# Kernel optimization log

Hardware: AMD Instinct MI355X
Metric: run time of the kernel (lower is better)

Reference implementation:

```python
import jax, jax.numpy as jnp
from jax import lax
import numpy as np

RATIOS = (0.5, 1.0, 2.0)
SCALES = (8, 16, 32)
BASE = 16
STRIDE = 16
IMG_H, IMG_W = 1024, 1024
NMS_THR = 0.7
N_IN = 6000   # eval mode (training=False)
N_OUT = 300
MIN_SIZE = 16


def _base_anchors():
    ctr = BASE / 2.0
    anc = []
    for r in RATIOS:
        for s in SCALES:
            h = BASE * s * np.sqrt(r)
            w = BASE * s * np.sqrt(1.0 / r)
            anc.append([ctr - h / 2, ctr - w / 2, ctr + h / 2, ctr + w / 2])
    return np.asarray(anc, dtype=np.float32)  # (9,4) yxyx


def _shifted_anchors(H, W):
    base = _base_anchors()
    sy = np.arange(H, dtype=np.float32) * STRIDE
    sx = np.arange(W, dtype=np.float32) * STRIDE
    yy, xx = np.meshgrid(sy, sx, indexing='ij')
    shift = np.stack([yy, xx, yy, xx], axis=-1).reshape(-1, 1, 4)  # (H*W,1,4)
    return jnp.asarray((shift + base[None]).reshape(-1, 4))        # (H*W*9,4)


def _conv(x, w, b):
    y = lax.conv_general_dilated(x, w, (1, 1), 'SAME',
                                 dimension_numbers=('NCHW', 'OIHW', 'NCHW'))
    return y + b[None, :, None, None]


def _loc2bbox(src, locs):
    h = src[:, 2] - src[:, 0]
    w = src[:, 3] - src[:, 1]
    cy = src[:, 0] + 0.5 * h
    cx = src[:, 1] + 0.5 * w
    dy, dx, dh, dw = locs[:, 0], locs[:, 1], locs[:, 2], locs[:, 3]
    cty = dy * h + cy
    ctx = dx * w + cx
    th = jnp.exp(dh) * h
    tw = jnp.exp(dw) * w
    return jnp.stack([cty - 0.5 * th, ctx - 0.5 * tw,
                      cty + 0.5 * th, ctx + 0.5 * tw], axis=-1)


def _nms_keep(boxes, valid):
    n = boxes.shape[0]
    areas = (boxes[:, 2] - boxes[:, 0]) * (boxes[:, 3] - boxes[:, 1])
    idx = jnp.arange(n)

    def body(i, keep):
        b = lax.dynamic_slice(boxes, (i, 0), (1, 4))[0]
        yy1 = jnp.maximum(b[0], boxes[:, 0])
        xx1 = jnp.maximum(b[1], boxes[:, 1])
        yy2 = jnp.minimum(b[2], boxes[:, 2])
        xx2 = jnp.minimum(b[3], boxes[:, 3])
        inter = jnp.clip(yy2 - yy1, 0) * jnp.clip(xx2 - xx1, 0)
        iou = inter / (areas[i] + areas - inter + 1e-9)
        sup = (iou > NMS_THR) & (idx > i) & keep[i]
        return keep & ~sup

    return lax.fori_loop(0, n, body, valid)


def _proposals(locs, fg, anchors):
    # locs (R,4), fg (R,), anchors (R,4) -> (N_OUT,4) padded with zeros
    rois = _loc2bbox(anchors, locs)
    y1 = jnp.clip(rois[:, 0], 0, IMG_H)
    y2 = jnp.clip(rois[:, 2], 0, IMG_H)
    x1 = jnp.clip(rois[:, 1], 0, IMG_W)
    x2 = jnp.clip(rois[:, 3], 0, IMG_W)
    rois = jnp.stack([y1, x1, y2, x2], axis=-1)
    valid = ((y2 - y1) >= MIN_SIZE) & ((x2 - x1) >= MIN_SIZE)
    s = jnp.where(valid, fg, -jnp.inf)
    order = jnp.argsort(-s)[:N_IN]
    rois_s = rois[order]
    valid_s = valid[order]
    keep = _nms_keep(rois_s, valid_s)
    rank = jnp.cumsum(keep.astype(jnp.int32)) - 1
    tgt = jnp.where(keep & (rank < N_OUT), rank, N_OUT)
    out = jnp.zeros((N_OUT + 1, 4), rois.dtype).at[tgt].set(rois_s)
    return out[:N_OUT]


def reference(x, conv_w, conv_b, score_w, score_b, loc_w, loc_b):
    B, C, H, W = x.shape
    anchors = _shifted_anchors(H, W)                      # (R,4)
    h = jax.nn.relu(_conv(x, conv_w, conv_b))             # (B,mid,H,W)
    rpn_locs = _conv(h, loc_w, loc_b).transpose(0, 2, 3, 1).reshape(B, -1, 4)
    rpn_scores = _conv(h, score_w, score_b).transpose(0, 2, 3, 1).reshape(B, -1, 2)
    fg = jax.nn.softmax(rpn_scores, axis=2)[:, :, 1]      # (B,R)
    rois = jax.vmap(_proposals, in_axes=(0, 0, None))(rpn_locs, fg, anchors)
    rois = rois.reshape(-1, 4)                            # (B*N_OUT,4)
    roi_indices = jnp.repeat(jnp.arange(B, dtype=jnp.int32), N_OUT)
    return rpn_scores, rpn_locs, rois, roi_indices, anchors


def setup_inputs() -> dict:
    key = jax.random.key(0)
    ks = jax.random.split(key, 7)
    B, Cin, Cmid, H, W = 4, 512, 512, 64, 64
    return {
        'x': jax.random.normal(ks[0], (B, Cin, H, W), jnp.float32),
        'conv_w': jax.random.normal(ks[1], (Cmid, Cin, 3, 3), jnp.float32) * 0.01,
        'conv_b': jax.random.normal(ks[2], (Cmid,), jnp.float32) * 0.01,
        'score_w': jax.random.normal(ks[3], (18, Cmid, 1, 1), jnp.float32) * 0.01,
        'score_b': jax.random.normal(ks[4], (18,), jnp.float32) * 0.01,
        'loc_w': jax.random.normal(ks[5], (36, Cmid, 1, 1), jnp.float32) * 0.01,
        'loc_b': jax.random.normal(ks[6], (36,), jnp.float32) * 0.01,
    }
```

## Files before the change

### kernel.cpp

```cpp
#include <hip/hip_runtime.h>
#include <cstdint>
#include <cmath>

namespace {
constexpr int BATCH = 4;
constexpr int CIN   = 512;
constexpr int CMID  = 512;
constexpr int HSZ   = 64, WSZ = 64, HWP = 4096;
constexpr int NA    = 36864;
constexpr int NIN_  = 6000;
constexpr int NOUT2 = 300;
constexpr int NW    = 94;

constexpr size_t O_SC  = 0;
constexpr size_t O_LC  = 294912;
constexpr size_t O_ROI = 884736;
constexpr size_t O_IDX = 889536;
constexpr size_t O_ANC = 890736;

constexpr size_t W_H    = 0;
constexpr size_t W_WHI  = 8388608;
constexpr size_t W_XSP  = 10747904;
constexpr size_t W_END_PS = 19136512;
constexpr size_t W_R4   = 0;
constexpr size_t W_SK   = 589824;
constexpr size_t W_CNT  = 753664;
constexpr size_t W_GH0  = 753728;
constexpr size_t W_GH1  = 770112;
constexpr size_t W_CT0  = 786496;
constexpr size_t W_CKEY = 901184;
constexpr size_t W_RS   = 1196096;
constexpr size_t W_VS   = 1292096;
constexpr size_t W_MAT  = 1316096;
}

typedef _Float16 f16;
typedef __attribute__((ext_vector_type(4))) _Float16 f16x4;
typedef __attribute__((ext_vector_type(8))) _Float16 f16x8;
typedef __attribute__((ext_vector_type(4))) float f32x4;

__global__ __launch_bounds__(256) void k0w(const float* __restrict__ w,
                                           f16* __restrict__ gw2) {
    int g = blockIdx.x * 256 + threadIdx.x;
    int lane = g & 63;
    int t1 = g >> 6;
    int hl = t1 & 1;
    int nt = (t1 >> 1) & 3;
    int wc = (t1 >> 3) & 1;
    int cg = (t1 >> 4) & 3;
    int ck = t1 >> 6;
    int kk = ck % 9;
    int chunk = ck / 9;
    int co  = cg * 128 + wc * 64 + nt * 16 + (lane & 15);
    int ci0 = chunk * 32 + (lane >> 4) * 8;
    f16x8 o;
#pragma unroll
    for (int e = 0; e < 8; ++e) {
        float f = w[((size_t)co * CIN + ci0 + e) * 9 + kk] * 64.0f;
        f16 hv = (f16)f;
        o[e] = hl ? (f16)((f - (float)hv) * 2048.0f) : hv;
    }
    *(f16x8*)&gw2[(size_t)g * 8] = o;
}

__global__ __launch_bounds__(256) void k0x(const float* __restrict__ x,
                                           f16* __restrict__ xsp) {
    const int pt = blockIdx.x, ch = blockIdx.y, b = blockIdx.z, t = threadIdx.x;
    __shared__ float ld[32 * 261];
    const int px0 = pt * 256;
    const int lpx = (t & 63) * 4, lc0 = t >> 6;
#pragma unroll
    for (int r = 0; r < 8; ++r) {
        int ci = r * 4 + lc0;
        float4 v = *(const float4*)&x[((size_t)(b * 512 + ch * 32 + ci)) * 4096 + px0 + lpx];
        float* d = &ld[ci * 261 + lpx];
        d[0] = v.x; d[1] = v.y; d[2] = v.z; d[3] = v.w;
    }
    __syncthreads();
    size_t ob = ((size_t)(b * 16 + ch) * 4096 + px0 + t) * 64;
#pragma unroll
    for (int cqx = 0; cqx < 8; ++cqx) {
        f16x8 o;
#pragma unroll
        for (int i = 0; i < 4; ++i) {
            float f = ld[(cqx * 4 + i) * 261 + t];
            f16 hf = (f16)f;
            o[i]     = hf;
            o[4 + i] = (f16)((f - (float)hf) * 2048.0f);
        }
        *(f16x8*)&xsp[ob + cqx * 8] = o;
    }
}

template <bool PS>
__global__ __launch_bounds__(256, 2) void k1_mfma(const float* __restrict__ x,
                                                  const f16* __restrict__ xsp,
                                                  const f16* __restrict__ gw2,
                                                  const float* __restrict__ bias,
                                                  float* __restrict__ h) {
    const int pt = blockIdx.x, cg = blockIdx.y, b = blockIdx.z;
    const int y0 = pt * 2, co0 = cg * 128;
    const int t = threadIdx.x;
    const int wave = t >> 6, lane = t & 63;
    const int wp = wave >> 1, wc = wave & 1;
    const int m = lane & 15, q = lane >> 4;

    __shared__ __align__(16) f16 xs[2][4 * 66 * 40];

    f32x4 acc1[2][2][4], acc2[2][2][4];
#pragma unroll
    for (int r = 0; r < 2; ++r)
#pragma unroll
        for (int j = 0; j < 2; ++j)
#pragma unroll
            for (int n = 0; n < 4; ++n) { acc1[r][j][n] = (f32x4)0.0f; acc2[r][j][n] = (f32x4)0.0f; }

    const int cq = t & 7, srow = (t >> 3) & 3, cseg = t >> 5;
    const int gy = y0 - 1 + srow;
    const bool yok = (gy >= 0 && gy < HSZ);

    if (t < 128) {
        int buf = t >> 6, rr = (t >> 4) & 3, cc = ((t >> 3) & 1) ? 65 : 0, cq2 = t & 7;
        f16x4 z = (f16x4)(f16)0.0f;
        *(f16x4*)&xs[buf][(rr * 66 + cc) * 40 + cq2 * 4] = z;
    }

    const size_t wlanebase = (size_t)(cg * 2 + wc) * 4096 + (size_t)lane * 8;

    f16x8 xv[8];
    if (PS) {
        const f16* xb = xsp + (((size_t)(b * 16 + 0) * 4096 + (size_t)(yok ? gy : 0) * 64) * 64);
#pragma unroll
        for (int jj = 0; jj < 8; ++jj) {
            int c = (jj + cq) & 7;
            xv[jj] = (f16x8)(f16)0.0f;
            if (yok) xv[jj] = *(const f16x8*)&xb[(size_t)(cseg * 8 + c) * 64 + cq * 8];
        }
    }

    for (int chunk = 0; chunk < 16; ++chunk) {
        __syncthreads();
        if (PS) {
#pragma unroll
            for (int jj = 0; jj < 8; ++jj) {
                int c = (jj + cq) & 7;
                int col = cseg * 8 + c + 1;
                f16x8 v = xv[jj];
                int base = (srow * 66 + col) * 40 + cq * 4;
                *(f16x4*)&xs[0][base] = __builtin_shufflevector(v, v, 0, 1, 2, 3);
                *(f16x4*)&xs[1][base] = __builtin_shufflevector(v, v, 4, 5, 6, 7);
            }
        } else {
            float vbuf[4][8];
            const float* xp = x + ((size_t)(b * CIN + chunk * 32 + cq * 4)) * HWP + gy * WSZ + cseg * 8;
#pragma unroll
            for (int i = 0; i < 4; ++i) {
                if (yok) {
                    float4 u0 = *(const float4*)(xp + (size_t)i * HWP);
                    float4 u1 = *(const float4*)(xp + (size_t)i * HWP + 4);
                    vbuf[i][0] = u0.x; vbuf[i][1] = u0.y; vbuf[i][2] = u0.z; vbuf[i][3] = u0.w;
                    vbuf[i][4] = u1.x; vbuf[i][5] = u1.y; vbuf[i][6] = u1.z; vbuf[i][7] = u1.w;
                } else {
#pragma unroll
                    for (int jj = 0; jj < 8; ++jj) vbuf[i][jj] = 0.0f;
                }
            }
#pragma unroll
            for (int jj = 0; jj < 8; ++jj) {
                int c = (jj + cq) & 7;
                int col = cseg * 8 + c + 1;
                f16x4 hv, lv;
#pragma unroll
                for (int i = 0; i < 4; ++i) {
                    float f = vbuf[i][c];
                    f16 hf = (f16)f;
                    hv[i] = hf;
                    lv[i] = (f16)((f - (float)hf) * 2048.0f);
                }
                int base = (srow * 66 + col) * 40 + cq * 4;
                *(f16x4*)&xs[0][base] = hv;
                *(f16x4*)&xs[1][base] = lv;
            }
        }
        __syncthreads();

        if (PS && chunk + 1 < 16) {
            const f16* xb2 = xsp + (((size_t)(b * 16 + chunk + 1) * 4096 + (size_t)(yok ? gy : 0) * 64) * 64);
#pragma unroll
            for (int jj = 0; jj < 8; ++jj) {
                int c = (jj + cq) & 7;
                xv[jj] = (f16x8)(f16)0.0f;
                if (yok) xv[jj] = *(const f16x8*)&xb2[(size_t)(cseg * 8 + c) * 64 + cq * 8];
            }
        }

        const f16* wck = gw2 + (size_t)chunk * (9 * 32768) + wlanebase;
#pragma unroll
        for (int kk = 0; kk < 9; ++kk) {
            const int ky = (kk >= 6) ? 2 : (kk >= 3) ? 1 : 0;
            const int kx = kk - ky * 3;
            const f16* wptr = wck + (size_t)kk * 32768;
            f16x8 bh[4], bl[4];
#pragma unroll
            for (int nt = 0; nt < 4; ++nt) {
                bh[nt] = *(const f16x8*)&wptr[nt * 1024];
                bl[nt] = *(const f16x8*)&wptr[nt * 1024 + 512];
            }
            f16x8 ah[2][2], al[2][2];
#pragma unroll
            for (int r = 0; r < 2; ++r)
#pragma unroll
                for (int j = 0; j < 2; ++j) {
                    int off = ((r + ky) * 66 + (wp * 2 + j) * 16 + m + kx) * 40 + q * 8;
                    ah[r][j] = *(const f16x8*)&xs[0][off];
                    al[r][j] = *(const f16x8*)&xs[1][off];
                }
#pragma unroll
            for (int r = 0; r < 2; ++r)
#pragma unroll
                for (int j = 0; j < 2; ++j)
#pragma unroll
                    for (int nt = 0; nt < 4; ++nt) {
                        acc1[r][j][nt] = __builtin_amdgcn_mfma_f32_16x16x32_f16(ah[r][j], bh[nt], acc1[r][j][nt], 0, 0, 0);
                        acc2[r][j][nt] = __builtin_amdgcn_mfma_f32_16x16x32_f16(ah[r][j], bl[nt], acc2[r][j][nt], 0, 0, 0);
                        acc2[r][j][nt] = __builtin_amdgcn_mfma_f32_16x16x32_f16(al[r][j], bh[nt], acc2[r][j][nt], 0, 0, 0);
                    }
        }
    }

#pragma unroll
    for (int r = 0; r < 2; ++r) {
        const int y = y0 + r;
#pragma unroll
        for (int nt = 0; nt < 4; ++nt) {
            const int co = co0 + wc * 64 + nt * 16 + m;
            const float bv = bias[co];
            size_t rowbase = ((size_t)(b * CMID + co)) * HWP + y * WSZ;
#pragma unroll
            for (int j = 0; j < 2; ++j) {
                float4 o;
                o.x = fmaxf((acc1[r][j][nt][0] + acc2[r][j][nt][0] * (1.0f / 2048.0f)) * (1.0f / 64.0f) + bv, 0.0f);
                o.y = fmaxf((acc1[r][j][nt][1] + acc2[r][j][nt][1] * (1.0f / 2048.0f)) * (1.0f / 64.0f) + bv, 0.0f);
                o.z = fmaxf((acc1[r][j][nt][2] + acc2[r][j][nt][2] * (1.0f / 2048.0f)) * (1.0f / 64.0f) + bv, 0.0f);
                o.w = fmaxf((acc1[r][j][nt][3] + acc2[r][j][nt][3] * (1.0f / 2048.0f)) * (1.0f / 64.0f) + bv, 0.0f);
                *(float4*)&h[rowbase + (wp * 2 + j) * 16 + q * 4] = o;
            }
        }
    }
}

__global__ __launch_bounds__(256) void k2_conv1(const float* __restrict__ h,
                                                const float* __restrict__ sw,
                                                const float* __restrict__ sb,
                                                const float* __restrict__ lw,
                                                const float* __restrict__ lb,
                                                float* __restrict__ out) {
    const int y = blockIdx.x;
    const int b = blockIdx.y;
    const int t = threadIdx.x;
    const int c4  = (t & 15) * 4;
    const int px4 = (t >> 4) * 4;
    __shared__ __align__(16) float hs[1024];
    __shared__ __align__(16) float wsm[16 * 68];

    float acc[4][4];
#pragma unroll
    for (int i = 0; i < 4; ++i)
#pragma unroll
        for (int j = 0; j < 4; ++j) acc[i][j] = 0.f;

    const int s_px = (t & 15) * 4;
    const int s_ci = t >> 4;
    for (int ci0 = 0; ci0 < CMID; ci0 += 16) {
        *(float4*)&hs[s_ci * 64 + s_px] =
            *(const float4*)&h[((size_t)(b * CMID + ci0 + s_ci)) * HWP + y * 64 + s_px];
#pragma unroll
        for (int k = 0; k < 4; ++k) {
            int idx = k * 256 + t;
            int ci = idx & 15, c = idx >> 4;
            float v = 0.f;
            if (c < 18) v = sw[c * 512 + ci0 + ci];
            else if (c < 54) v = lw[(c - 18) * 512 + ci0 + ci];
            wsm[ci * 68 + c] = v;
        }
        __syncthreads();
#pragma unroll
        for (int ci = 0; ci < 16; ++ci) {
            float4 hv = *(const float4*)&hs[ci * 64 + px4];
            float4 wv = *(const float4*)&wsm[ci * 68 + c4];
            acc[0][0] = fmaf(wv.x, hv.x, acc[0][0]);
            acc[0][1] = fmaf(wv.x, hv.y, acc[0][1]);
            acc[0][2] = fmaf(wv.x, hv.z, acc[0][2]);
            acc[0][3] = fmaf(wv.x, hv.w, acc[0][3]);
            acc[1][0] = fmaf(wv.y, hv.x, acc[1][0]);
            acc[1][1] = fmaf(wv.y, hv.y, acc[1][1]);
            acc[1][2] = fmaf(wv.y, hv.z, acc[1][2]);
            acc[1][3] = fmaf(wv.y, hv.w, acc[1][3]);
            acc[2][0] = fmaf(wv.z, hv.x, acc[2][0]);
            acc[2][1] = fmaf(wv.z, hv.y, acc[2][1]);
            acc[2][2] = fmaf(wv.z, hv.z, acc[2][2]);
            acc[2][3] = fmaf(wv.z, hv.w, acc[2][3]);
            acc[3][0] = fmaf(wv.w, hv.x, acc[3][0]);
            acc[3][1] = fmaf(wv.w, hv.y, acc[3][1]);
            acc[3][2] = fmaf(wv.w, hv.z, acc[3][2]);
            acc[3][3] = fmaf(wv.w, hv.w, acc[3][3]);
        }
        __syncthreads();
    }

#pragma unroll
    for (int cc = 0; cc < 4; ++cc) {
        int c = c4 + cc;
        if (c >= 54) break;
        float bv = (c < 18) ? sb[c] : lb[c - 18];
#pragma unroll
        for (int pp = 0; pp < 4; ++pp) {
            int px = y * 64 + px4 + pp;
            float v = acc[cc][pp] + bv;
            if (c < 18)
                out[O_SC + (size_t)b * 73728 + (size_t)px * 18 + c] = v;
            else
                out[O_LC + (size_t)b * 147456 + (size_t)px * 36 + (c - 18)] = v;
        }
    }
}

__global__ __launch_bounds__(256) void k4z(int* __restrict__ gh,
                                           int* __restrict__ gcnt) {
    int i = blockIdx.x * 256 + threadIdx.x;
    gh[i] = 0;
    if (i < BATCH) gcnt[i] = 0;
}

__global__ __launch_bounds__(256) void k3_prop(float* __restrict__ out,
                                               float* __restrict__ rois4,
                                               float* __restrict__ skey,
                                               int* __restrict__ gh0) {
    const int t = threadIdx.x;
    const int p = blockIdx.x * 256 + t;
    const int b = blockIdx.y;
    __shared__ int lh[4096];
    for (int k = t; k < 4096; k += 256) lh[k] = 0;
    __syncthreads();
    const int px = p / 9;
    const int a  = p - px * 9;
    const int yy = px >> 6, xx = px & 63;
    const int ri = a / 3, si = a - ri * 3;
    const double rat[3] = {0.5, 1.0, 2.0};
    const double scl[3] = {8.0, 16.0, 32.0};
    double hhd = 16.0 * scl[si] * sqrt(rat[ri]);
    double wwd = 16.0 * scl[si] * sqrt(1.0 / rat[ri]);
    float a0 = (float)(8.0 - hhd / 2.0), a1 = (float)(8.0 - wwd / 2.0);
    float a2 = (float)(8.0 + hhd / 2.0), a3 = (float)(8.0 + wwd / 2.0);
    float sy = (float)(yy * 16), sx = (float)(xx * 16);
    float A0 = sy + a0, A1 = sx + a1, A2 = sy + a2, A3 = sx + a3;
    if (b == 0) {
        float4 av; av.x = A0; av.y = A1; av.z = A2; av.w = A3;
        *(float4*)&out[O_ANC + (size_t)p * 4] = av;
    }
    const float* sc = out + O_SC + (size_t)b * 73728 + (size_t)px * 18 + a * 2;
    float s0 = sc[0], s1 = sc[1];
    float mm = fmaxf(s0, s1);
    float e0 = expf(s0 - mm), e1 = expf(s1 - mm);
    float fg = e1 / (e0 + e1);
    const float* lc = out + O_LC + (size_t)b * 147456 + (size_t)px * 36 + a * 4;
    float dy = lc[0], dxv = lc[1], dh = lc[2], dwv = lc[3];
    float ah = A2 - A0, aw = A3 - A1;
    float cy = A0 + 0.5f * ah, cx = A1 + 0.5f * aw;
    float cty = dy * ah + cy, ctx = dxv * aw + cx;
    float th = expf(dh) * ah, tw = expf(dwv) * aw;
    float ry1 = cty - 0.5f * th, rx1 = ctx - 0.5f * tw;
    float ry2 = cty + 0.5f * th, rx2 = ctx + 0.5f * tw;
    float y1 = fminf(fmaxf(ry1, 0.f), 1024.f);
    float y2 = fminf(fmaxf(ry2, 0.f), 1024.f);
    float x1 = fminf(fmaxf(rx1, 0.f), 1024.f);
    float x2 = fminf(fmaxf(rx2, 0.f), 1024.f);
    bool valid = ((y2 - y1) >= 16.f) && ((x2 - x1) >= 16.f);
    float sk = valid ? fg : -__builtin_inff();
    float4 rv; rv.x = y1; rv.y = x1; rv.z = y2; rv.w = x2;
    *(float4*)&rois4[((size_t)b * NA + p) * 4] = rv;
    skey[(size_t)b * NA + p] = sk;
    unsigned uu = __float_as_uint(sk);
    uu = (uu & 0x80000000u) ? ~uu : (uu | 0x80000000u);
    atomicAdd(&lh[uu >> 20], 1);
    __syncthreads();
    for (int k = t; k < 4096; k += 256) {
        int v = lh[k];
        if (v) atomicAdd(&gh0[(size_t)b * 4096 + k], v);
    }
}

__global__ __launch_bounds__(256) void k4cut0(const int* __restrict__ gh,
                                              int* __restrict__ cut0,
                                              int* __restrict__ prev0) {
    const int b = blockIdx.x, t = threadIdx.x;
    __shared__ int hh[4096];
    __shared__ int tsum[256];
    __shared__ int s_cut, s_prev;
    for (int k = t; k < 4096; k += 256) hh[k] = gh[(size_t)b * 4096 + k];
    __syncthreads();
    int s = 0;
#pragma unroll
    for (int j = 0; j < 16; ++j) s += hh[t * 16 + j];
    tsum[t] = s;
    __syncthreads();
    if (t == 0) {
        int run = 0;
        for (int tt = 255; tt >= 0; --tt) { int tmp = tsum[tt]; tsum[tt] = run; run += tmp; }
    }
    __syncthreads();
    {
        const int target = NIN_;
        int run = tsum[t];
        for (int v = t * 16 + 15; v >= t * 16; --v) {
            int prev = run;
            run += hh[v];
            if (run >= target && prev < target) { s_cut = v; s_prev = prev; }
        }
    }
    __syncthreads();
    if (t == 0) { cut0[b] = s_cut; prev0[b] = s_prev; }
}

__global__ __launch_bounds__(256) void k4h1(const float* __restrict__ skey,
                                            const int* __restrict__ cut0,
                                            int* __restrict__ gh1,
                                            float* __restrict__ rois_s,
                                            int* __restrict__ valid_s) {
    const int b = blockIdx.y, t = threadIdx.x;
    {
        int gid = (blockIdx.y * 32 + blockIdx.x) * 256 + t;
        if (gid < BATCH * NIN_) valid_s[gid] = 0;
        for (int k = gid; k < BATCH * NIN_ * 4; k += 32768) rois_s[k] = 0.f;
    }
    __shared__ int lh[4096];
    for (int k = t; k < 4096; k += 256) lh[k] = 0;
    __syncthreads();
    const int c1 = cut0[b];
    for (int i = blockIdx.x * 256 + t; i < NA; i += 32 * 256) {
        float sk = skey[(size_t)b * NA + i];
        unsigned u = __float_as_uint(sk);
        u = (u & 0x80000000u) ? ~u : (u | 0x80000000u);
        if ((int)(u >> 20) == c1) atomicAdd(&lh[(u >> 8) & 0xFFFu], 1);
    }
    __syncthreads();
    for (int k = t; k < 4096; k += 256) {
        int v = lh[k];
        if (v) atomicAdd(&gh1[(size_t)b * 4096 + k], v);
    }
}

__global__ __launch_bounds__(256) void k4cut1(const int* __restrict__ gh,
                                              const int* __restrict__ prev0,
                                              int* __restrict__ cut1) {
    const int b = blockIdx.x, t = threadIdx.x;
    __shared__ int hh[4096];
    __shared__ int tsum[256];
    __shared__ int s_cut;
    for (int k = t; k < 4096; k += 256) hh[k] = gh[(size_t)b * 4096 + k];
    __syncthreads();
    int s = 0;
#pragma unroll
    for (int j = 0; j < 16; ++j) s += hh[t * 16 + j];
    tsum[t] = s;
    __syncthreads();
    if (t == 0) {
        int run = 0;
        for (int tt = 255; tt >= 0; --tt) { int tmp = tsum[tt]; tsum[tt] = run; run += tmp; }
    }
    __syncthreads();
    {
        const int target = NIN_ - prev0[b];
        int run = tsum[t];
        for (int v = t * 16 + 15; v >= t * 16; --v) {
            int prev = run;
            run += hh[v];
            if (run >= target && prev < target) { s_cut = v; }
        }
    }
    __syncthreads();
    if (t == 0) cut1[b] = s_cut;
}

__global__ __launch_bounds__(256) void k4cmp(const float* __restrict__ skey,
                                             const int* __restrict__ cut0,
                                             const int* __restrict__ cut1,
                                             int* __restrict__ gcnt,
                                             unsigned long long* __restrict__ ckey) {
    const int b = blockIdx.y, t = threadIdx.x;
    __shared__ unsigned long long lbuf[1280];
    __shared__ int lcnt, lbase;
    if (t == 0) lcnt = 0;
    __syncthreads();
    const int c1 = cut0[b], c2 = cut1[b];
    for (int i = blockIdx.x * 256 + t; i < NA; i += 32 * 256) {
        float sk = skey[(size_t)b * NA + i];
        unsigned u = __float_as_uint(sk);
        u = (u & 0x80000000u) ? ~u : (u | 0x80000000u);
        int b1 = (int)(u >> 20), b2 = (int)((u >> 8) & 0xFFFu);
        if (b1 > c1 || (b1 == c1 && b2 >= c2)) {
            int lp = atomicAdd(&lcnt, 1);
            lbuf[lp] = ((unsigned long long)u << 16) | (unsigned long long)(36863 - i);
        }
    }
    __syncthreads();
    if (t == 0) lbase = atomicAdd(gcnt + b, lcnt);
    __syncthreads();
    const int n = lcnt, base = lbase;
    for (int k = t; k < n; k += 256) ckey[(size_t)b * NA + base + k] = lbuf[k];
}

__global__ __launch_bounds__(256) void k4d_rank(const int* __restrict__ cnt,
                                                const unsigned long long* __restrict__ ckey,
                                                const float* __restrict__ rois4,
                                                float* __restrict__ rois_s,
                                                int* __restrict__ valid_s) {
    const int b = blockIdx.y;
    const int C = cnt[b];
    if (blockIdx.x * 256 >= C) return;
    const int gi = blockIdx.x * 256 + threadIdx.x;
    const bool act = gi < C;
    const unsigned long long mk = act ? ckey[(size_t)b * NA + gi] : 0ULL;
    __shared__ unsigned long long kl[512];
    int rank = 0;
    for (int c0 = 0; c0 < C; c0 += 512) {
        __syncthreads();
#pragma unroll
        for (int kk = 0; kk < 2; ++kk) {
            int k = threadIdx.x + kk * 256;
            int src = c0 + k;
            kl[k] = (src < C) ? ckey[(size_t)b * NA + src] : 0ULL;
        }
        __syncthreads();
        if (act) {
            int n = min(512, C - c0);
            int j = 0;
            for (; j + 4 <= n; j += 4) {
                rank += (kl[j]     > mk);
                rank += (kl[j + 1] > mk);
                rank += (kl[j + 2] > mk);
                rank += (kl[j + 3] > mk);
            }
            for (; j < n; ++j) rank += (kl[j] > mk);
        }
    }
    if (act && rank < NIN_) {
        int p = 36863 - (int)(mk & 0xFFFFull);
        const float4 bx = *(const float4*)&rois4[((size_t)b * NA + p) * 4];
        *(float4*)&rois_s[((size_t)b * NIN_ + rank) * 4] = bx;
        valid_s[b * NIN_ + rank] = ((unsigned)(mk >> 16) != 0x007FFFFFu) ? 1 : 0;
    }
}

__global__ __launch_bounds__(256) void k5_mat(const float* __restrict__ rois_s,
                                              unsigned long long* __restrict__ mat) {
    const int b = blockIdx.y, rb = blockIdx.x;
    const int t = threadIdx.x, wave = t >> 6, lane = t & 63;
    const int i = rb * 64 + lane;
    const bool rowok = (i < NIN_);
    __shared__ float cs[4][5][64];
    const float* bb = rois_s + (size_t)b * NIN_ * 4;

    float r0 = 0, r1 = 0, r2 = 0, r3 = 0, ra = 0;
    if (rowok) {
        float4 v = *(const float4*)&bb[(size_t)i * 4];
        r0 = v.x; r1 = v.y; r2 = v.z; r3 = v.w;
        ra = (v.z - v.x) * (v.w - v.y);
    }
    unsigned long long* mrow = mat + ((size_t)b * NIN_ + (size_t)(rowok ? i : 0)) * NW;

    if (rowok)
        for (int cb = wave; cb < rb; cb += 4) mrow[cb] = 0ull;

    for (int cb = rb + wave; cb < NW; cb += 4) {
        const int j0 = cb * 64;
        const int j  = j0 + lane;
        float4 v;
        if (j < NIN_) v = *(const float4*)&bb[(size_t)j * 4];
        else { v.x = 0; v.y = 0; v.z = 0; v.w = 0; }
        cs[wave][0][lane] = v.x; cs[wave][1][lane] = v.y;
        cs[wave][2][lane] = v.z; cs[wave][3][lane] = v.w;
        cs[wave][4][lane] = (v.z - v.x) * (v.w - v.y);
        unsigned long long wm = 0;
        if (rowok) {
#pragma unroll 8
            for (int k = 0; k < 64; ++k) {
                float yy1 = fmaxf(r0, cs[wave][0][k]), xx1 = fmaxf(r1, cs[wave][1][k]);
                float yy2 = fminf(r2, cs[wave][2][k]), xx2 = fminf(r3, cs[wave][3][k]);
                float inter = fmaxf(yy2 - yy1, 0.f) * fmaxf(xx2 - xx1, 0.f);
                float iou = inter / (ra + cs[wave][4][k] - inter + 1e-9f);
                int jj = j0 + k;
                if ((iou > 0.7f) && (jj > i) && (jj < NIN_)) wm |= (1ull << k);
            }
            mrow[cb] = wm;
        }
    }
}

__global__ __launch_bounds__(64) void k5_scan(const unsigned long long* __restrict__ mat,
                                              const float* __restrict__ rois_s,
                                              const int* __restrict__ valid_s,
                                              float* __restrict__ out) {
    const int b = blockIdx.x, t = threadIdx.x;
    for (int k = t; k < NOUT2 * 4; k += 64) out[O_ROI + (size_t)b * NOUT2 * 4 + k] = 0.f;
    for (int k = t; k < NOUT2; k += 64) out[O_IDX + (size_t)b * NOUT2 + k] = (float)b;

    unsigned long long A = 0, B = 0;
    for (int w = 0; w < NW; ++w) {
        int i = w * 64 + t;
        int v = (i < NIN_) ? valid_s[b * NIN_ + i] : 0;
        unsigned long long m = __ballot(v == 0);
        if (w < 64) { if (t == w) A = m; }
        else        { if (t == w - 64) B = m; }
    }

    const unsigned long long* mb = mat + (size_t)b * NIN_ * NW;
    const float* bb = rois_s + (size_t)b * NIN_ * 4;
    int kept = 0;
    for (int w = 0; w < NW && kept < NOUT2; ++w) {
        unsigned long long cur = (w < 64) ? __shfl(A, w) : __shfl(B, w - 64);
        unsigned long long avail = ~cur;
        while (avail != 0ull && kept < NOUT2) {
            int b0 = __builtin_ctzll(avail);
            unsigned long long rest = avail & (avail - 1ull);
            const int i0 = w * 64 + b0;
            const unsigned long long* row0 = mb + (size_t)i0 * NW;
            unsigned long long r0A = row0[t];
            unsigned long long r0B = (t < NW - 64) ? row0[64 + t] : 0ull;
            const bool has1 = (rest != 0ull);
            const int b1 = has1 ? __builtin_ctzll(rest) : 0;
            unsigned long long r1A = 0ull, r1B = 0ull;
            if (has1) {
                const unsigned long long* row1 = mb + (size_t)(w * 64 + b1) * NW;
                r1A = row1[t];
                r1B = (t < NW - 64) ? row1[64 + t] : 0ull;
            }
            if (t == 0) {
                float4 bx = *(const float4*)&bb[(size_t)i0 * 4];
                *(float4*)&out[O_ROI + ((size_t)b * NOUT2 + kept) * 4] = bx;
            }
            kept++;
            if (kept >= NOUT2) break;
            A |= r0A; B |= r0B;
            unsigned long long rw0 = (w < 64) ? __shfl(r0A, w) : __shfl(r0B, w - 64);
            avail &= ~rw0;
            avail &= ~(1ull << b0);
            if (has1 && (avail & (1ull << b1))) {
                if (t == 0) {
                    float4 bx = *(const float4*)&bb[(size_t)(w * 64 + b1) * 4];
                    *(float4*)&out[O_ROI + ((size_t)b * NOUT2 + kept) * 4] = bx;
                }
                kept++;
                if (kept >= NOUT2) break;
                A |= r1A; B |= r1B;
                unsigned long long rw1 = (w < 64) ? __shfl(r1A, w) : __shfl(r1B, w - 64);
                avail &= ~rw1;
                avail &= ~(1ull << b1);
            }
        }
    }
}

extern "C" void kernel_launch(void* const* d_in, const int* in_sizes, int n_in,
                              void* d_out, int out_size, void* d_ws, size_t ws_size,
                              hipStream_t stream) {
    const float* x       = (const float*)d_in[0];
    const float* conv_w  = (const float*)d_in[1];
    const float* conv_b  = (const float*)d_in[2];
    const float* score_w = (const float*)d_in[3];
    const float* score_b = (const float*)d_in[4];
    const float* loc_w   = (const float*)d_in[5];
    const float* loc_b   = (const float*)d_in[6];
    float* out = (float*)d_out;
    float* ws  = (float*)d_ws;

    f16* gw2 = (f16*)(ws + W_WHI);
    f16* xsp = (f16*)(ws + W_XSP);
    int* gcnt = (int*)(ws + W_CNT);
    int* gh0  = (int*)(ws + W_GH0);
    int* gh1  = (int*)(ws + W_GH1);
    int* ct0  = (int*)(ws + W_CT0);
    int* pv0  = ct0 + BATCH;
    int* ct1  = pv0 + BATCH;
    unsigned long long* ckey = (unsigned long long*)(ws + W_CKEY);
    const bool ps = (ws_size >= (size_t)W_END_PS * 4);

    k0w<<<589824 / 256, 256, 0, stream>>>(conv_w, gw2);
    if (ps) {
        k0x<<<dim3(16, 16, 4), 256, 0, stream>>>(x, xsp);
        k1_mfma<true><<<dim3(32, 4, 4), 256, 0, stream>>>(x, xsp, gw2, conv_b, ws + W_H);
    } else {
        k1_mfma<false><<<dim3(32, 4, 4), 256, 0, stream>>>(x, nullptr, gw2, conv_b, ws + W_H);
    }
    k2_conv1<<<dim3(64, 4), 256, 0, stream>>>(ws + W_H, score_w, score_b, loc_w, loc_b, out);
    k4z<<<128, 256, 0, stream>>>(gh0, gcnt);
    k3_prop<<<dim3(144, 4), 256, 0, stream>>>(out, ws + W_R4, ws + W_SK, gh0);
    k4cut0<<<BATCH, 256, 0, stream>>>(gh0, ct0, pv0);
    k4h1<<<dim3(32, BATCH), 256, 0, stream>>>(ws + W_SK, ct0, gh1, ws + W_RS,
                                              (int*)(ws + W_VS));
    k4cut1<<<BATCH, 256, 0, stream>>>(gh1, pv0, ct1);
    k4cmp<<<dim3(32, BATCH), 256, 0, stream>>>(ws + W_SK, ct0, ct1, gcnt, ckey);
    k4d_rank<<<dim3(144, BATCH), 256, 0, stream>>>(gcnt, ckey, ws + W_R4, ws + W_RS,
                                                   (int*)(ws + W_VS));
    k5_mat<<<dim3(NW, BATCH), 256, 0, stream>>>(ws + W_RS, (unsigned long long*)(ws + W_MAT));
    k5_scan<<<BATCH, 64, 0, stream>>>((const unsigned long long*)(ws + W_MAT),
                                      ws + W_RS, (const int*)(ws + W_VS), out);
}
```

Measured before the change: 867.1 us.

## Drop second radix pass, fuse zeroing into conv1, remove x prefetch

The proposal top-k selection no longer runs a second-level histogram and cut kernel. Instead, compaction keeps every key whose top 12-bit bucket is at or above the first cut, which leaves more candidates for the rank kernel to sort. Histogram and counter zeroing moves from a separate kernel into k2_conv1, with the histogram now placed in the dead weight-buffer region. Together these remove three launches and their serialization. In the main MFMA conv, the register double-buffered prefetch of the fp16 input is dropped in favour of direct loads at each chunk, trading load/compute overlap for lower register pressure.

New measurement: 1.089 ms. 25.6% more time.

```diff
diff --git a/kernel.cpp b/kernel.cpp
--- a/kernel.cpp
+++ b/kernel.cpp
@@ -20,13 +20,12 @@
 
 constexpr size_t W_H    = 0;
 constexpr size_t W_WHI  = 8388608;
+constexpr size_t W_GH0  = 8388608;
+constexpr size_t W_GCNT = 8404992;
 constexpr size_t W_XSP  = 10747904;
 constexpr size_t W_END_PS = 19136512;
 constexpr size_t W_R4   = 0;
 constexpr size_t W_SK   = 589824;
-constexpr size_t W_CNT  = 753664;
-constexpr size_t W_GH0  = 753728;
-constexpr size_t W_GH1  = 770112;
 constexpr size_t W_CT0  = 786496;
 constexpr size_t W_CKEY = 901184;
 constexpr size_t W_RS   = 1196096;
@@ -127,25 +126,16 @@
 
     const size_t wlanebase = (size_t)(cg * 2 + wc) * 4096 + (size_t)lane * 8;
 
-    f16x8 xv[8];
-    if (PS) {
-        const f16* xb = xsp + (((size_t)(b * 16 + 0) * 4096 + (size_t)(yok ? gy : 0) * 64) * 64);
-#pragma unroll
-        for (int jj = 0; jj < 8; ++jj) {
-            int c = (jj + cq) & 7;
-            xv[jj] = (f16x8)(f16)0.0f;
-            if (yok) xv[jj] = *(const f16x8*)&xb[(size_t)(cseg * 8 + c) * 64 + cq * 8];
-        }
-    }
-
     for (int chunk = 0; chunk < 16; ++chunk) {
         __syncthreads();
         if (PS) {
+            const f16* xb = xsp + (((size_t)(b * 16 + chunk) * 4096 + (size_t)(yok ? gy : 0) * 64) * 64);
 #pragma unroll
             for (int jj = 0; jj < 8; ++jj) {
                 int c = (jj + cq) & 7;
                 int col = cseg * 8 + c + 1;
-                f16x8 v = xv[jj];
+                f16x8 v = (f16x8)(f16)0.0f;
+                if (yok) v = *(const f16x8*)&xb[(size_t)(cseg * 8 + c) * 64 + cq * 8];
                 int base = (srow * 66 + col) * 40 + cq * 4;
                 *(f16x4*)&xs[0][base] = __builtin_shufflevector(v, v, 0, 1, 2, 3);
                 *(f16x4*)&xs[1][base] = __builtin_shufflevector(v, v, 4, 5, 6, 7);
@@ -184,16 +174,6 @@
         }
         __syncthreads();
 
-        if (PS && chunk + 1 < 16) {
-            const f16* xb2 = xsp + (((size_t)(b * 16 + chunk + 1) * 4096 + (size_t)(yok ? gy : 0) * 64) * 64);
-#pragma unroll
-            for (int jj = 0; jj < 8; ++jj) {
-                int c = (jj + cq) & 7;
-                xv[jj] = (f16x8)(f16)0.0f;
-                if (yok) xv[jj] = *(const f16x8*)&xb2[(size_t)(cseg * 8 + c) * 64 + cq * 8];
-            }
-        }
-
         const f16* wck = gw2 + (size_t)chunk * (9 * 32768) + wlanebase;
 #pragma unroll
         for (int kk = 0; kk < 9; ++kk) {
@@ -254,10 +234,17 @@
                                                 const float* __restrict__ sb,
                                                 const float* __restrict__ lw,
                                                 const float* __restrict__ lb,
-                                                float* __restrict__ out) {
+                                                float* __restrict__ out,
+                                                int* __restrict__ gz,
+                                                int* __restrict__ gcnt) {
     const int y = blockIdx.x;
     const int b = blockIdx.y;
     const int t = threadIdx.x;
+    {
+        int fb = (blockIdx.y * 64 + blockIdx.x) * 256 + t;
+        if (fb < 4096 * BATCH) gz[fb] = 0;
+        if (fb < BATCH) gcnt[fb] = 0;
+    }
     const int c4  = (t & 15) * 4;
     const int px4 = (t >> 4) * 4;
     __shared__ __align__(16) float hs[1024];
@@ -323,13 +310,6 @@
                 out[O_LC + (size_t)b * 147456 + (size_t)px * 36 + (c - 18)] = v;
         }
     }
-}
-
-__global__ __launch_bounds__(256) void k4z(int* __restrict__ gh,
-                                           int* __restrict__ gcnt) {
-    int i = blockIdx.x * 256 + threadIdx.x;
-    gh[i] = 0;
-    if (i < BATCH) gcnt[i] = 0;
 }
 
 __global__ __launch_bounds__(256) void k3_prop(float* __restrict__ out,
@@ -422,83 +402,28 @@
     if (t == 0) { cut0[b] = s_cut; prev0[b] = s_prev; }
 }
 
-__global__ __launch_bounds__(256) void k4h1(const float* __restrict__ skey,
-                                            const int* __restrict__ cut0,
-                                            int* __restrict__ gh1,
-                                            float* __restrict__ rois_s,
-                                            int* __restrict__ valid_s) {
+__global__ __launch_bounds__(256) void k4cmp(const float* __restrict__ skey,
+                                             const int* __restrict__ cut0,
+                                             int* __restrict__ gcnt,
+                                             unsigned long long* __restrict__ ckey,
+                                             float* __restrict__ rois_s,
+                                             int* __restrict__ valid_s) {
     const int b = blockIdx.y, t = threadIdx.x;
     {
         int gid = (blockIdx.y * 32 + blockIdx.x) * 256 + t;
         if (gid < BATCH * NIN_) valid_s[gid] = 0;
         for (int k = gid; k < BATCH * NIN_ * 4; k += 32768) rois_s[k] = 0.f;
     }
-    __shared__ int lh[4096];
-    for (int k = t; k < 4096; k += 256) lh[k] = 0;
+    __shared__ unsigned long long lbuf[1280];
+    __shared__ int lcnt, lbase;
+    if (t == 0) lcnt = 0;
     __syncthreads();
     const int c1 = cut0[b];
     for (int i = blockIdx.x * 256 + t; i < NA; i += 32 * 256) {
         float sk = skey[(size_t)b * NA + i];
         unsigned u = __float_as_uint(sk);
         u = (u & 0x80000000u) ? ~u : (u | 0x80000000u);
-        if ((int)(u >> 20) == c1) atomicAdd(&lh[(u >> 8) & 0xFFFu], 1);
-    }
-    __syncthreads();
-    for (int k = t; k < 4096; k += 256) {
-        int v = lh[k];
-        if (v) atomicAdd(&gh1[(size_t)b * 4096 + k], v);
-    }
-}
-
-__global__ __launch_bounds__(256) void k4cut1(const int* __restrict__ gh,
-                                              const int* __restrict__ prev0,
-                                              int* __restrict__ cut1) {
-    const int b = blockIdx.x, t = threadIdx.x;
-    __shared__ int hh[4096];
-    __shared__ int tsum[256];
-    __shared__ int s_cut;
-    for (int k = t; k < 4096; k += 256) hh[k] = gh[(size_t)b * 4096 + k];
-    __syncthreads();
-    int s = 0;
-#pragma unroll
-    for (int j = 0; j < 16; ++j) s += hh[t * 16 + j];
-    tsum[t] = s;
-    __syncthreads();
-    if (t == 0) {
-        int run = 0;
-        for (int tt = 255; tt >= 0; --tt) { int tmp = tsum[tt]; tsum[tt] = run; run += tmp; }
-    }
-    __syncthreads();
-    {
-        const int target = NIN_ - prev0[b];
-        int run = tsum[t];
-        for (int v = t * 16 + 15; v >= t * 16; --v) {
-            int prev = run;
-            run += hh[v];
-            if (run >= target && prev < target) { s_cut = v; }
-        }
-    }
-    __syncthreads();
-    if (t == 0) cut1[b] = s_cut;
-}
-
-__global__ __launch_bounds__(256) void k4cmp(const float* __restrict__ skey,
-                                             const int* __restrict__ cut0,
-                                             const int* __restrict__ cut1,
-                                             int* __restrict__ gcnt,
-                                             unsigned long long* __restrict__ ckey) {
-    const int b = blockIdx.y, t = threadIdx.x;
-    __shared__ unsigned long long lbuf[1280];
-    __shared__ int lcnt, lbase;
-    if (t == 0) lcnt = 0;
-    __syncthreads();
-    const int c1 = cut0[b], c2 = cut1[b];
-    for (int i = blockIdx.x * 256 + t; i < NA; i += 32 * 256) {
-        float sk = skey[(size_t)b * NA + i];
-        unsigned u = __float_as_uint(sk);
-        u = (u & 0x80000000u) ? ~u : (u | 0x80000000u);
-        int b1 = (int)(u >> 20), b2 = (int)((u >> 8) & 0xFFFu);
-        if (b1 > c1 || (b1 == c1 && b2 >= c2)) {
+        if ((int)(u >> 20) >= c1) {
             int lp = atomicAdd(&lcnt, 1);
             lbuf[lp] = ((unsigned long long)u << 16) | (unsigned long long)(36863 - i);
         }
@@ -676,12 +601,10 @@
 
     f16* gw2 = (f16*)(ws + W_WHI);
     f16* xsp = (f16*)(ws + W_XSP);
-    int* gcnt = (int*)(ws + W_CNT);
     int* gh0  = (int*)(ws + W_GH0);
-    int* gh1  = (int*)(ws + W_GH1);
+    int* gcnt = (int*)(ws + W_GCNT);
     int* ct0  = (int*)(ws + W_CT0);
     int* pv0  = ct0 + BATCH;
-    int* ct1  = pv0 + BATCH;
     unsigned long long* ckey = (unsigned long long*)(ws + W_CKEY);
     const bool ps = (ws_size >= (size_t)W_END_PS * 4);
 
@@ -692,14 +615,12 @@
     } else {
         k1_mfma<false><<<dim3(32, 4, 4), 256, 0, stream>>>(x, nullptr, gw2, conv_b, ws + W_H);
     }
-    k2_conv1<<<dim3(64, 4), 256, 0, stream>>>(ws + W_H, score_w, score_b, loc_w, loc_b, out);
-    k4z<<<128, 256, 0, stream>>>(gh0, gcnt);
+    k2_conv1<<<dim3(64, 4), 256, 0, stream>>>(ws + W_H, score_w, score_b, loc_w, loc_b, out,
+                                              gh0, gcnt);
     k3_prop<<<dim3(144, 4), 256, 0, stream>>>(out, ws + W_R4, ws + W_SK, gh0);
     k4cut0<<<BATCH, 256, 0, stream>>>(gh0, ct0, pv0);
-    k4h1<<<dim3(32, BATCH), 256, 0, stream>>>(ws + W_SK, ct0, gh1, ws + W_RS,
-                                              (int*)(ws + W_VS));
-    k4cut1<<<BATCH, 256, 0, stream>>>(gh1, pv0, ct1);
-    k4cmp<<<dim3(32, BATCH), 256, 0, stream>>>(ws + W_SK, ct0, ct1, gcnt, ckey);
+    k4cmp<<<dim3(32, BATCH), 256, 0, stream>>>(ws + W_SK, ct0, gcnt, ckey,
+                                               ws + W_RS, (int*)(ws + W_VS));
     k4d_rank<<<dim3(144, BATCH), 256, 0, stream>>>(gcnt, ckey, ws + W_R4, ws + W_RS,
                                                    (int*)(ws + W_VS));
     k5_mat<<<dim3(NW, BATCH), 256, 0, stream>>>(ws + W_RS, (unsigned long long*)(ws + W_MAT));
```
